# Kernel optimization log

Measured on AMD Instinct MI355X. Metric: run time of the kernel, lower is better.

## Reference

```python
import jax, jax.numpy as jnp
import numpy as np

NEG_SLOPE = 0.2  # PyG GATv2Conv default leaky_relu slope
N_NODES = 50000
N_EDGES = 800000
F_IN = 128
HID = 32
HEADS = 4
OUT_HEADS = 1
N_CLS = 16
MLP_HID = 128


def topk_mask(score, dst, k, num_nodes):
    """Boolean mask [E,H]: True where edge score is among top-k for its destination."""
    E = score.shape[0]
    counts = jnp.zeros((num_nodes,), jnp.int32).at[dst].add(1)
    starts = jnp.cumsum(counts) - counts  # first sorted index of each dst segment

    def one_head(s):
        o1 = jnp.argsort(-s)                       # sort by score desc
        o2 = jnp.argsort(dst[o1], stable=True)     # stable sort by dst -> (dst asc, score desc)
        perm = o1[o2]
        rank = jnp.arange(E) - starts[dst[perm]]   # rank within dst segment
        return jnp.zeros((E,), bool).at[perm].set(rank < k)

    return jax.vmap(one_head, in_axes=1, out_axes=1)(score)


def masked_segment_softmax(score, mask, dst, num_nodes):
    neg = jnp.where(mask, score, -jnp.inf)
    m = jax.ops.segment_max(neg, dst, num_segments=num_nodes)
    m = jnp.where(jnp.isfinite(m), m, 0.0)
    ex = jnp.where(mask, jnp.exp(score - m[dst]), 0.0)
    s = jax.ops.segment_sum(ex, dst, num_segments=num_nodes)
    return ex / (s[dst] + 1e-16)


def gatv2_topk(x, edge_index, k, Wl, Wr, att, b, heads, out_c, concat, num_nodes):
    src, dst = edge_index[0], edge_index[1]
    xl = (x @ Wl).reshape(num_nodes, heads, out_c)
    xr = (x @ Wr).reshape(num_nodes, heads, out_c)
    h = xl[src] + xr[dst]                                   # [E,H,C]
    e = jnp.einsum('ehc,hc->eh', jax.nn.leaky_relu(h, NEG_SLOPE), att)  # [E,H]
    keep = topk_mask(e, dst, k, num_nodes)
    alpha = masked_segment_softmax(e, keep, dst, num_nodes)       # top-k attention
    alpha_n = masked_segment_softmax(e, ~keep, dst, num_nodes)    # truncated (noise) attention
    msg = xl[src]                                                  # [E,H,C]
    out = jax.ops.segment_sum(alpha[..., None] * msg, dst, num_segments=num_nodes)
    noise = jax.ops.segment_sum(alpha_n[..., None] * msg, dst, num_segments=num_nodes)
    if concat:
        out = out.reshape(num_nodes, heads * out_c)
        noise = noise.reshape(num_nodes, heads * out_c)
    else:
        out = out.mean(axis=1)
        noise = noise.mean(axis=1)
    return out + b, noise + b


def setup_inputs() -> dict:
    key = jax.random.key(0)
    ks = jax.random.split(key, 14)
    s = 0.1
    x = jax.random.normal(ks[0], (N_NODES, F_IN), jnp.float32)
    edge_index = jax.random.randint(ks[1], (2, N_EDGES), 0, N_NODES, dtype=jnp.int64)
    return {
        'x': x,
        'edge_index': edge_index,
        'attn_topk': 8,
        'Wl1': jax.random.normal(ks[2], (F_IN, HEADS * HID), jnp.float32) * s,
        'Wr1': jax.random.normal(ks[3], (F_IN, HEADS * HID), jnp.float32) * s,
        'att1': jax.random.normal(ks[4], (HEADS, HID), jnp.float32) * s,
        'b1': jnp.zeros((HEADS * HID,), jnp.float32),
        'Wl2': jax.random.normal(ks[5], (HEADS * HID, OUT_HEADS * N_CLS), jnp.float32) * s,
        'Wr2': jax.random.normal(ks[6], (HEADS * HID, OUT_HEADS * N_CLS), jnp.float32) * s,
        'att2': jax.random.normal(ks[7], (OUT_HEADS, N_CLS), jnp.float32) * s,
        'b2': jnp.zeros((N_CLS,), jnp.float32),
        'lin1_w': jax.random.normal(ks[8], (HEADS * HID, MLP_HID), jnp.float32) * s,
        'lin1_b': jnp.zeros((MLP_HID,), jnp.float32),
        'lin2_w': jax.random.normal(ks[9], (MLP_HID, N_CLS), jnp.float32) * s,
        'lin2_b': jnp.zeros((N_CLS,), jnp.float32),
    }


def reference(x, edge_index, attn_topk, Wl1, Wr1, att1, b1, Wl2, Wr2, att2, b2,
              lin1_w, lin1_b, lin2_w, lin2_b):
    # eval mode: dropout is identity
    h, noise1 = gatv2_topk(x, edge_index, attn_topk, Wl1, Wr1, att1, b1,
                           HEADS, HID, True, N_NODES)
    h = jax.nn.elu(h)
    n1 = jax.nn.elu(noise1 @ lin1_w + lin1_b) @ lin2_w + lin2_b
    out, noise2 = gatv2_topk(h, edge_index, attn_topk, Wl2, Wr2, att2, b2,
                             OUT_HEADS, N_CLS, False, N_NODES)
    return (jax.nn.log_softmax(out, axis=1),
            jax.nn.log_softmax(n1, axis=1),
            jax.nn.log_softmax(noise2, axis=1))
```

## Files before the change

kernel.cpp:

```cpp
#include <hip/hip_runtime.h>
#include <math.h>

#define NN 50000
#define NE 800000
#define FIN 128
#define HEADS 4
#define HID 32
#define D1 128
#define NCLS 16
#define NEG 0.2f
#define NINF (-3.402823466e38f)
#define CAP 64
#define SB 256
#define NSB ((NN + SB - 1) / SB)

__global__ void k_count(const int* __restrict__ dst, int* __restrict__ counts) {
  int j = blockIdx.x * 256 + threadIdx.x;
  if (j < NE) atomicAdd(&counts[dst[j]], 1);
}

__global__ void k_scanA(const int* __restrict__ counts, int* __restrict__ bsum) {
  int b = blockIdx.x, t = threadIdx.x;
  int idx = b * SB + t;
  int v = idx < NN ? counts[idx] : 0;
  __shared__ int ws[4];
#pragma unroll
  for (int o = 1; o <= 32; o <<= 1) v += __shfl_xor(v, o, 64);
  if ((t & 63) == 0) ws[t >> 6] = v;
  __syncthreads();
  if (t == 0) bsum[b] = ws[0] + ws[1] + ws[2] + ws[3];
}

__global__ void k_scanB(const int* __restrict__ bsum, int* __restrict__ boff) {
  int t = threadIdx.x;
  int v = t < NSB ? bsum[t] : 0;
  __shared__ int tmp[256];
  tmp[t] = v;
  __syncthreads();
  for (int o = 1; o < 256; o <<= 1) {
    int u = t >= o ? tmp[t - o] : 0;
    __syncthreads();
    tmp[t] += u;
    __syncthreads();
  }
  if (t < NSB) boff[t] = tmp[t] - v;
}

__global__ void k_scanC(const int* __restrict__ counts, const int* __restrict__ boff,
                        int* __restrict__ starts, int* __restrict__ cursor) {
  int b = blockIdx.x, t = threadIdx.x;
  int idx = b * SB + t;
  int v = idx < NN ? counts[idx] : 0;
  __shared__ int tmp[256];
  tmp[t] = v;
  __syncthreads();
  for (int o = 1; o < 256; o <<= 1) {
    int u = t >= o ? tmp[t - o] : 0;
    __syncthreads();
    tmp[t] += u;
    __syncthreads();
  }
  int ex = tmp[t] - v + boff[b];
  if (idx < NN) { starts[idx] = ex; cursor[idx] = ex; }
}

__global__ void k_scatter(const int* __restrict__ src, const int* __restrict__ dst,
                          int* __restrict__ cursor, int* __restrict__ eperm,
                          int* __restrict__ sperm) {
  int j = blockIdx.x * 256 + threadIdx.x;
  if (j < NE) {
    int p = atomicAdd(&cursor[dst[j]], 1);
    eperm[p] = j;
    sperm[p] = src[j];
  }
}

template <int BM, int BN, int BK, int TM, int TN, int ACT>
__global__ __launch_bounds__(256) void k_gemm(const float* __restrict__ A,
                                              const float* __restrict__ B,
                                              const float* __restrict__ bias,
                                              float* __restrict__ C, int M, int N, int K) {
  constexpr int NT = (BM / TM) * (BN / TN);
  static_assert(NT == 256, "block must be 256 threads");
  __shared__ float As[BK][BM + 4];
  __shared__ float Bs[BK][BN];
  int tid = threadIdx.x;
  int bm = blockIdx.y * BM, bn = blockIdx.x * BN;
  constexpr int TX = BN / TN;
  int tn = (tid % TX) * TN;
  int tm = (tid / TX) * TM;
  float acc[TM][TN];
#pragma unroll
  for (int i = 0; i < TM; i++)
#pragma unroll
    for (int j = 0; j < TN; j++) acc[i][j] = 0.f;

  for (int k0 = 0; k0 < K; k0 += BK) {
    constexpr int AV = BM * BK / 4;
    for (int i = tid; i < AV; i += NT) {
      int r = i / (BK / 4);
      int c4 = (i % (BK / 4)) * 4;
      float4 v = make_float4(0.f, 0.f, 0.f, 0.f);
      int gr = bm + r;
      if (gr < M) v = *(const float4*)(A + (size_t)gr * K + k0 + c4);
      As[c4 + 0][r] = v.x; As[c4 + 1][r] = v.y; As[c4 + 2][r] = v.z; As[c4 + 3][r] = v.w;
    }
    constexpr int BV = BK * BN / 4;
    for (int i = tid; i < BV; i += NT) {
      int r = i / (BN / 4), c4 = (i % (BN / 4)) * 4;
      float4 v = *(const float4*)(B + (size_t)(k0 + r) * N + bn + c4);
      Bs[r][c4 + 0] = v.x; Bs[r][c4 + 1] = v.y; Bs[r][c4 + 2] = v.z; Bs[r][c4 + 3] = v.w;
    }
    __syncthreads();
#pragma unroll
    for (int kk = 0; kk < BK; kk++) {
      float ra[TM], rb[TN];
#pragma unroll
      for (int i = 0; i < TM; i++) ra[i] = As[kk][tm + i];
#pragma unroll
      for (int j = 0; j < TN; j++) rb[j] = Bs[kk][tn + j];
#pragma unroll
      for (int i = 0; i < TM; i++)
#pragma unroll
        for (int j = 0; j < TN; j++) acc[i][j] += ra[i] * rb[j];
    }
    __syncthreads();
  }
#pragma unroll
  for (int i = 0; i < TM; i++) {
    int gr = bm + tm + i;
    if (gr >= M) continue;
#pragma unroll
    for (int j = 0; j < TN; j++) {
      float v = acc[i][j];
      if (bias) v += bias[bn + tn + j];
      if (ACT == 1) v = v > 0.f ? v : expm1f(v);
      C[(size_t)gr * N + bn + tn + j] = v;
    }
  }
}

__device__ __forceinline__ bool lex_gt(float av, int ai, float bv, int bi) {
  return (av > bv) || (av == bv && ai < bi);
}

__global__ __launch_bounds__(256) void k_fused1(
    const float* __restrict__ xl, const float* __restrict__ xr,
    const float* __restrict__ att, const int* __restrict__ sperm,
    const int* __restrict__ eperm, const int* __restrict__ starts,
    const int* __restrict__ counts, const int* __restrict__ kptr,
    const float* __restrict__ bias, float* __restrict__ hout,
    float* __restrict__ nout) {
  __shared__ float sc[4][CAP][4];
  int w = threadIdx.x >> 6;
  int l = threadIdx.x & 63;
  int d = blockIdx.x * 4 + w;
  if (d >= NN) return;
  int st = starts[d];
  int deg = counts[d];
  if (deg > CAP) deg = CAP;
  int k = kptr[0];

  int srcreg = 0, idreg = 0x7fffffff;
  if (l < deg) { srcreg = sperm[st + l]; idreg = eperm[st + l]; }

  int h2 = l >> 5, li = l & 31;
  int headq = li >> 3;
  float4 xrv = *(const float4*)(xr + (size_t)d * D1 + 4 * li);
  float4 attv = *(const float4*)(att + 4 * li);
  float4 b1v = *(const float4*)(bias + 4 * li);

  for (int q = 0; q < deg; q += 4) {
    int r0 = q + h2, r1 = q + 2 + h2;
    int s0 = __shfl(srcreg, r0), s1 = __shfl(srcreg, r1);
    bool v0 = r0 < deg, v1 = r1 < deg;
    float4 x0 = make_float4(0.f, 0.f, 0.f, 0.f), x1 = x0;
    if (v0) x0 = *(const float4*)(xl + (size_t)s0 * D1 + 4 * li);
    if (v1) x1 = *(const float4*)(xl + (size_t)s1 * D1 + 4 * li);
    float a0, a1, p0 = 0.f, p1 = 0.f;
    a0 = x0.x + xrv.x; p0 += (a0 > 0.f ? a0 : NEG * a0) * attv.x;
    a0 = x0.y + xrv.y; p0 += (a0 > 0.f ? a0 : NEG * a0) * attv.y;
    a0 = x0.z + xrv.z; p0 += (a0 > 0.f ? a0 : NEG * a0) * attv.z;
    a0 = x0.w + xrv.w; p0 += (a0 > 0.f ? a0 : NEG * a0) * attv.w;
    a1 = x1.x + xrv.x; p1 += (a1 > 0.f ? a1 : NEG * a1) * attv.x;
    a1 = x1.y + xrv.y; p1 += (a1 > 0.f ? a1 : NEG * a1) * attv.y;
    a1 = x1.z + xrv.z; p1 += (a1 > 0.f ? a1 : NEG * a1) * attv.z;
    a1 = x1.w + xrv.w; p1 += (a1 > 0.f ? a1 : NEG * a1) * attv.w;
#pragma unroll
    for (int o = 1; o <= 4; o <<= 1) {
      p0 += __shfl_xor(p0, o, 64);
      p1 += __shfl_xor(p1, o, 64);
    }
    if ((li & 7) == 0) {
      if (v0) sc[w][r0][headq] = p0;
      if (v1) sc[w][r1][headq] = p1;
    }
  }

  int hh = l >> 4, ii = l & 15;
  float sv[4]; int si[4]; int rank[4]; bool val[4];
#pragma unroll
  for (int j = 0; j < 4; j++) {
    int q = j * 16 + ii;
    val[j] = q < deg;
    sv[j] = val[j] ? sc[w][q][hh] : NINF;
    int bid = __shfl(idreg, q);
    si[j] = val[j] ? bid : 0x7fffffff;
    rank[j] = 0;
  }
#pragma unroll
  for (int ch = 0; ch < 4; ch++) {
    if (ch * 16 >= deg) break;
#pragma unroll
    for (int pp = 0; pp < 16; pp++) {
      int p = ch * 16 + pp;
      float bv = __shfl(sv[ch], hh * 16 + pp);
      int bi = __shfl(si[ch], hh * 16 + pp);
      if (p < deg) {
#pragma unroll
        for (int j = 0; j < 4; j++) rank[j] += lex_gt(bv, bi, sv[j], si[j]);
      }
    }
  }
  bool kept[4];
#pragma unroll
  for (int j = 0; j < 4; j++) kept[j] = val[j] && (rank[j] < k);
  float mk = fmaxf(fmaxf(sv[0], sv[1]), fmaxf(sv[2], sv[3]));
  float mn = NINF;
#pragma unroll
  for (int j = 0; j < 4; j++) mn = fmaxf(mn, kept[j] ? NINF : sv[j]);
#pragma unroll
  for (int o = 1; o <= 8; o <<= 1) {
    mk = fmaxf(mk, __shfl_xor(mk, o, 64));
    mn = fmaxf(mn, __shfl_xor(mn, o, 64));
  }
  float ek[4], en[4], sk = 0.f, sn = 0.f;
#pragma unroll
  for (int j = 0; j < 4; j++) {
    ek[j] = kept[j] ? __expf(sv[j] - mk) : 0.f;
    en[j] = (val[j] && !kept[j]) ? __expf(sv[j] - mn) : 0.f;
    sk += ek[j]; sn += en[j];
  }
#pragma unroll
  for (int o = 1; o <= 8; o <<= 1) {
    sk += __shfl_xor(sk, o, 64);
    sn += __shfl_xor(sn, o, 64);
  }
  float ik = 1.f / (sk + 1e-16f), inn = 1.f / (sn + 1e-16f);
#pragma unroll
  for (int j = 0; j < 4; j++) {
    if (val[j]) sc[w][j * 16 + ii][hh] = kept[j] ? ek[j] * ik : -(en[j] * inn);
  }

  float4 ao = make_float4(0.f, 0.f, 0.f, 0.f), an = ao;
  for (int q = 0; q < deg; q += 4) {
    int r0 = q + h2, r1 = q + 2 + h2;
    int s0 = __shfl(srcreg, r0), s1 = __shfl(srcreg, r1);
    if (r0 < deg) {
      float wv = sc[w][r0][headq];
      float4 xv = *(const float4*)(xl + (size_t)s0 * D1 + 4 * li);
      float s = wv > 0.f ? wv : -wv;
      if (wv > 0.f) { ao.x += s * xv.x; ao.y += s * xv.y; ao.z += s * xv.z; ao.w += s * xv.w; }
      else          { an.x += s * xv.x; an.y += s * xv.y; an.z += s * xv.z; an.w += s * xv.w; }
    }
    if (r1 < deg) {
      float wv = sc[w][r1][headq];
      float4 xv = *(const float4*)(xl + (size_t)s1 * D1 + 4 * li);
      float s = wv > 0.f ? wv : -wv;
      if (wv > 0.f) { ao.x += s * xv.x; ao.y += s * xv.y; ao.z += s * xv.z; ao.w += s * xv.w; }
      else          { an.x += s * xv.x; an.y += s * xv.y; an.z += s * xv.z; an.w += s * xv.w; }
    }
  }
  ao.x += __shfl_xor(ao.x, 32, 64); ao.y += __shfl_xor(ao.y, 32, 64);
  ao.z += __shfl_xor(ao.z, 32, 64); ao.w += __shfl_xor(ao.w, 32, 64);
  an.x += __shfl_xor(an.x, 32, 64); an.y += __shfl_xor(an.y, 32, 64);
  an.z += __shfl_xor(an.z, 32, 64); an.w += __shfl_xor(an.w, 32, 64);
  if (h2 == 0) {
    float4 vo;
    vo.x = ao.x + b1v.x; vo.y = ao.y + b1v.y; vo.z = ao.z + b1v.z; vo.w = ao.w + b1v.w;
    vo.x = vo.x > 0.f ? vo.x : expm1f(vo.x);
    vo.y = vo.y > 0.f ? vo.y : expm1f(vo.y);
    vo.z = vo.z > 0.f ? vo.z : expm1f(vo.z);
    vo.w = vo.w > 0.f ? vo.w : expm1f(vo.w);
    *(float4*)(hout + (size_t)d * D1 + 4 * li) = vo;
  } else {
    float4 vn;
    vn.x = an.x + b1v.x; vn.y = an.y + b1v.y; vn.z = an.z + b1v.z; vn.w = an.w + b1v.w;
    *(float4*)(nout + (size_t)d * D1 + 4 * li) = vn;
  }
}

__global__ __launch_bounds__(256) void k_fused2(
    const float* __restrict__ xl, const float* __restrict__ xr,
    const float* __restrict__ att, const int* __restrict__ sperm,
    const int* __restrict__ eperm, const int* __restrict__ starts,
    const int* __restrict__ counts, const int* __restrict__ kptr,
    const float* __restrict__ bias, float* __restrict__ out0,
    float* __restrict__ out1) {
  __shared__ float sc[4][CAP];
  int w = threadIdx.x >> 6;
  int l = threadIdx.x & 63;
  int d = blockIdx.x * 4 + w;
  if (d >= NN) return;
  int st = starts[d];
  int deg = counts[d];
  if (deg > CAP) deg = CAP;
  int k = kptr[0];

  int srcreg = 0, idreg = 0x7fffffff;
  if (l < deg) { srcreg = sperm[st + l]; idreg = eperm[st + l]; }

  int g = l >> 4, li = l & 15;
  float xrv = xr[(size_t)d * NCLS + li];
  float attv = att[li];
  float bv2 = bias[li];

  for (int q = 0; q < deg; q += 8) {
    int r0 = q + g, r1 = q + 4 + g;
    int s0 = __shfl(srcreg, r0), s1 = __shfl(srcreg, r1);
    float x0 = (r0 < deg) ? xl[(size_t)s0 * NCLS + li] : 0.f;
    float x1 = (r1 < deg) ? xl[(size_t)s1 * NCLS + li] : 0.f;
    float a0 = x0 + xrv, a1 = x1 + xrv;
    float p0 = (a0 > 0.f ? a0 : NEG * a0) * attv;
    float p1 = (a1 > 0.f ? a1 : NEG * a1) * attv;
#pragma unroll
    for (int o = 1; o <= 8; o <<= 1) {
      p0 += __shfl_xor(p0, o, 64);
      p1 += __shfl_xor(p1, o, 64);
    }
    if (li == 0) {
      if (r0 < deg) sc[w][r0] = p0;
      if (r1 < deg) sc[w][r1] = p1;
    }
  }

  float sv = (l < deg) ? sc[w][l] : NINF;
  int si = idreg;
  int rank = 0;
  for (int p = 0; p < deg; p++) {
    float bv = __shfl(sv, p);
    int bi = __shfl(si, p);
    rank += lex_gt(bv, bi, sv, si);
  }
  bool kept = (l < deg) && (rank < k);
  float mk = sv, mn = kept ? NINF : sv;
#pragma unroll
  for (int o = 1; o <= 32; o <<= 1) {
    mk = fmaxf(mk, __shfl_xor(mk, o, 64));
    mn = fmaxf(mn, __shfl_xor(mn, o, 64));
  }
  float ek = kept ? __expf(sv - mk) : 0.f;
  float en = ((l < deg) && !kept) ? __expf(sv - mn) : 0.f;
  float sk = ek, sn = en;
#pragma unroll
  for (int o = 1; o <= 32; o <<= 1) {
    sk += __shfl_xor(sk, o, 64);
    sn += __shfl_xor(sn, o, 64);
  }
  if (l < deg) sc[w][l] = kept ? ek / (sk + 1e-16f) : -(en / (sn + 1e-16f));

  float ao = 0.f, an = 0.f;
  for (int q = 0; q < deg; q += 4) {
    int r = q + g;
    int s = __shfl(srcreg, r);
    if (r < deg) {
      float wv = sc[w][r];
      float xv = xl[(size_t)s * NCLS + li];
      if (wv > 0.f) ao += wv * xv; else an -= wv * xv;
    }
  }
  ao += __shfl_xor(ao, 16, 64); ao += __shfl_xor(ao, 32, 64);
  an += __shfl_xor(an, 16, 64); an += __shfl_xor(an, 32, 64);
  float vo = ao + bv2, vn = an + bv2;
  float mo = vo, mv = vn;
#pragma unroll
  for (int o = 1; o <= 8; o <<= 1) {
    mo = fmaxf(mo, __shfl_xor(mo, o, 64));
    mv = fmaxf(mv, __shfl_xor(mv, o, 64));
  }
  float eo = __expf(vo - mo), ev = __expf(vn - mv);
#pragma unroll
  for (int o = 1; o <= 8; o <<= 1) {
    eo += __shfl_xor(eo, o, 64);
    ev += __shfl_xor(ev, o, 64);
  }
  if (g == 0) out0[(size_t)d * NCLS + li] = vo - (mo + logf(eo));
  if (g == 1) out1[(size_t)d * NCLS + li] = vn - (mv + logf(ev));
}

__global__ void k_lsm(const float* __restrict__ in, float* __restrict__ out) {
  int r = blockIdx.x * 256 + threadIdx.x;
  if (r >= NN) return;
  const float4* p = (const float4*)(in + (size_t)r * NCLS);
  float4 a = p[0], b = p[1], c = p[2], d4 = p[3];
  float vals[16] = {a.x, a.y, a.z, a.w, b.x, b.y, b.z, b.w,
                    c.x, c.y, c.z, c.w, d4.x, d4.y, d4.z, d4.w};
  float m = vals[0];
#pragma unroll
  for (int i = 1; i < 16; i++) m = fmaxf(m, vals[i]);
  float s = 0.f;
#pragma unroll
  for (int i = 0; i < 16; i++) s += expf(vals[i] - m);
  float l = m + logf(s);
  float* op = out + (size_t)r * NCLS;
#pragma unroll
  for (int i = 0; i < 16; i++) op[i] = vals[i] - l;
}

extern "C" void kernel_launch(void* const* d_in, const int* in_sizes, int n_in,
                              void* d_out, int out_size, void* d_ws, size_t ws_size,
                              hipStream_t stream) {
  (void)in_sizes; (void)n_in; (void)out_size; (void)ws_size;
  const float* x    = (const float*)d_in[0];
  const int*   ei   = (const int*)d_in[1];
  const int*   kptr = (const int*)d_in[2];
  const float* Wl1  = (const float*)d_in[3];
  const float* Wr1  = (const float*)d_in[4];
  const float* att1 = (const float*)d_in[5];
  const float* b1   = (const float*)d_in[6];
  const float* Wl2  = (const float*)d_in[7];
  const float* Wr2  = (const float*)d_in[8];
  const float* att2 = (const float*)d_in[9];
  const float* b2   = (const float*)d_in[10];
  const float* l1w  = (const float*)d_in[11];
  const float* l1b  = (const float*)d_in[12];
  const float* l2w  = (const float*)d_in[13];
  const float* l2b  = (const float*)d_in[14];
  const int* srcv = ei;
  const int* dstv = ei + NE;

  char* wp = (char*)d_ws;
  auto alloc = [&](size_t n) { char* p = wp; wp += (n + 255) & ~(size_t)255; return p; };
  float* xl1    = (float*)alloc((size_t)NN * D1 * 4);
  float* bufB   = (float*)alloc((size_t)NN * D1 * 4);
  float* noise1 = (float*)alloc((size_t)NN * D1 * 4);
  float* t1     = (float*)alloc((size_t)NN * D1 * 4);
  int* counts = (int*)alloc((size_t)NN * 4);
  int* starts = (int*)alloc((size_t)NN * 4);
  int* cursor = (int*)alloc((size_t)NN * 4);
  int* eperm  = (int*)alloc((size_t)NE * 4);
  int* sperm  = (int*)alloc((size_t)NE * 4);
  int* bsum   = (int*)alloc((size_t)NSB * 4);
  int* boff   = (int*)alloc((size_t)NSB * 4);

  hipMemsetAsync(counts, 0, (size_t)NN * 4, stream);
  k_count<<<(NE + 255) / 256, 256, 0, stream>>>(dstv, counts);
  k_scanA<<<NSB, 256, 0, stream>>>(counts, bsum);
  k_scanB<<<1, 256, 0, stream>>>(bsum, boff);
  k_scanC<<<NSB, 256, 0, stream>>>(counts, boff, starts, cursor);
  k_scatter<<<(NE + 255) / 256, 256, 0, stream>>>(srcv, dstv, cursor, eperm, sperm);

  dim3 gbig(D1 / 64, (NN + 63) / 64);
  k_gemm<64, 64, 32, 4, 4, 0><<<gbig, 256, 0, stream>>>(x, Wl1, nullptr, xl1, NN, D1, FIN);
  k_gemm<64, 64, 32, 4, 4, 0><<<gbig, 256, 0, stream>>>(x, Wr1, nullptr, bufB, NN, D1, FIN);

  k_fused1<<<(NN + 3) / 4, 256, 0, stream>>>(xl1, bufB, att1, sperm, eperm,
                                             starts, counts, kptr, b1, bufB, noise1);

  k_gemm<64, 64, 32, 4, 4, 1><<<gbig, 256, 0, stream>>>(noise1, l1w, l1b, t1, NN, 128, 128);
  float* n1v = noise1;
  dim3 gsm(1, (NN + 127) / 128);
  k_gemm<128, 16, 32, 4, 2, 0><<<gsm, 256, 0, stream>>>(t1, l2w, l2b, n1v, NN, NCLS, 128);

  float* xl2 = t1;
  float* xr2 = t1 + (size_t)NN * NCLS;
  k_gemm<128, 16, 32, 4, 2, 0><<<gsm, 256, 0, stream>>>(bufB, Wl2, nullptr, xl2, NN, NCLS, D1);
  k_gemm<128, 16, 32, 4, 2, 0><<<gsm, 256, 0, stream>>>(bufB, Wr2, nullptr, xr2, NN, NCLS, D1);

  float* o = (float*)d_out;
  k_fused2<<<(NN + 3) / 4, 256, 0, stream>>>(xl2, xr2, att2, sperm, eperm, starts,
                                             counts, kptr, b2, o,
                                             o + (size_t)2 * NN * NCLS);

  k_lsm<<<(NN + 255) / 256, 256, 0, stream>>>(n1v, o + (size_t)NN * NCLS);
}
```

Baseline: 508.2 us.

## Fuse left/right projection GEMMs into one concatenated GEMM and vectorize fragments

```diff
diff --git a/kernel.cpp b/kernel.cpp
--- a/kernel.cpp
+++ b/kernel.cpp
@@ -76,12 +76,13 @@
 }
 
 template <int BM, int BN, int BK, int TM, int TN, int ACT>
-__global__ __launch_bounds__(256) void k_gemm(const float* __restrict__ A,
-                                              const float* __restrict__ B,
-                                              const float* __restrict__ bias,
-                                              float* __restrict__ C, int M, int N, int K) {
+__global__ __launch_bounds__(256) void k_gemm2(
+    const float* __restrict__ A, const float* __restrict__ B1,
+    const float* __restrict__ B2, int N1, int s1, int s2,
+    const float* __restrict__ bias, float* __restrict__ C, int M, int N, int K) {
   constexpr int NT = (BM / TM) * (BN / TN);
   static_assert(NT == 256, "block must be 256 threads");
+  static_assert(TM % 4 == 0 && TN % 4 == 0, "float4 fragments");
   __shared__ float As[BK][BM + 4];
   __shared__ float Bs[BK][BN];
   int tid = threadIdx.x;
@@ -108,7 +109,9 @@
     constexpr int BV = BK * BN / 4;
     for (int i = tid; i < BV; i += NT) {
       int r = i / (BN / 4), c4 = (i % (BN / 4)) * 4;
-      float4 v = *(const float4*)(B + (size_t)(k0 + r) * N + bn + c4);
+      int gc = bn + c4, gk = k0 + r;
+      float4 v = (gc < N1) ? *(const float4*)(B1 + (size_t)gk * s1 + gc)
+                           : *(const float4*)(B2 + (size_t)gk * s2 + (gc - N1));
       Bs[r][c4 + 0] = v.x; Bs[r][c4 + 1] = v.y; Bs[r][c4 + 2] = v.z; Bs[r][c4 + 3] = v.w;
     }
     __syncthreads();
@@ -116,9 +119,11 @@
     for (int kk = 0; kk < BK; kk++) {
       float ra[TM], rb[TN];
 #pragma unroll
-      for (int i = 0; i < TM; i++) ra[i] = As[kk][tm + i];
-#pragma unroll
-      for (int j = 0; j < TN; j++) rb[j] = Bs[kk][tn + j];
+      for (int i = 0; i < TM; i += 4)
+        *(float4*)&ra[i] = *(const float4*)&As[kk][tm + i];
+#pragma unroll
+      for (int j = 0; j < TN; j += 4)
+        *(float4*)&rb[j] = *(const float4*)&Bs[kk][tn + j];
 #pragma unroll
       for (int i = 0; i < TM; i++)
 #pragma unroll
@@ -131,11 +136,20 @@
     int gr = bm + tm + i;
     if (gr >= M) continue;
 #pragma unroll
-    for (int j = 0; j < TN; j++) {
-      float v = acc[i][j];
-      if (bias) v += bias[bn + tn + j];
-      if (ACT == 1) v = v > 0.f ? v : expm1f(v);
-      C[(size_t)gr * N + bn + tn + j] = v;
+    for (int j = 0; j < TN; j += 4) {
+      float4 v;
+      v.x = acc[i][j + 0]; v.y = acc[i][j + 1]; v.z = acc[i][j + 2]; v.w = acc[i][j + 3];
+      if (bias) {
+        v.x += bias[bn + tn + j + 0]; v.y += bias[bn + tn + j + 1];
+        v.z += bias[bn + tn + j + 2]; v.w += bias[bn + tn + j + 3];
+      }
+      if (ACT == 1) {
+        v.x = v.x > 0.f ? v.x : expm1f(v.x);
+        v.y = v.y > 0.f ? v.y : expm1f(v.y);
+        v.z = v.z > 0.f ? v.z : expm1f(v.z);
+        v.w = v.w > 0.f ? v.w : expm1f(v.w);
+      }
+      *(float4*)(C + (size_t)gr * N + bn + tn + j) = v;
     }
   }
 }
@@ -145,12 +159,11 @@
 }
 
 __global__ __launch_bounds__(256) void k_fused1(
-    const float* __restrict__ xl, const float* __restrict__ xr,
-    const float* __restrict__ att, const int* __restrict__ sperm,
-    const int* __restrict__ eperm, const int* __restrict__ starts,
-    const int* __restrict__ counts, const int* __restrict__ kptr,
-    const float* __restrict__ bias, float* __restrict__ hout,
-    float* __restrict__ nout) {
+    const float* __restrict__ xlr, const float* __restrict__ att,
+    const int* __restrict__ sperm, const int* __restrict__ eperm,
+    const int* __restrict__ starts, const int* __restrict__ counts,
+    const int* __restrict__ kptr, const float* __restrict__ bias,
+    float* __restrict__ hout, float* __restrict__ nout) {
   __shared__ float sc[4][CAP][4];
   int w = threadIdx.x >> 6;
   int l = threadIdx.x & 63;
@@ -166,34 +179,38 @@
 
   int h2 = l >> 5, li = l & 31;
   int headq = li >> 3;
-  float4 xrv = *(const float4*)(xr + (size_t)d * D1 + 4 * li);
+  float4 xrv = *(const float4*)(xlr + (size_t)d * 256 + 128 + 4 * li);
   float4 attv = *(const float4*)(att + 4 * li);
   float4 b1v = *(const float4*)(bias + 4 * li);
 
-  for (int q = 0; q < deg; q += 4) {
-    int r0 = q + h2, r1 = q + 2 + h2;
-    int s0 = __shfl(srcreg, r0), s1 = __shfl(srcreg, r1);
-    bool v0 = r0 < deg, v1 = r1 < deg;
-    float4 x0 = make_float4(0.f, 0.f, 0.f, 0.f), x1 = x0;
-    if (v0) x0 = *(const float4*)(xl + (size_t)s0 * D1 + 4 * li);
-    if (v1) x1 = *(const float4*)(xl + (size_t)s1 * D1 + 4 * li);
-    float a0, a1, p0 = 0.f, p1 = 0.f;
-    a0 = x0.x + xrv.x; p0 += (a0 > 0.f ? a0 : NEG * a0) * attv.x;
-    a0 = x0.y + xrv.y; p0 += (a0 > 0.f ? a0 : NEG * a0) * attv.y;
-    a0 = x0.z + xrv.z; p0 += (a0 > 0.f ? a0 : NEG * a0) * attv.z;
-    a0 = x0.w + xrv.w; p0 += (a0 > 0.f ? a0 : NEG * a0) * attv.w;
-    a1 = x1.x + xrv.x; p1 += (a1 > 0.f ? a1 : NEG * a1) * attv.x;
-    a1 = x1.y + xrv.y; p1 += (a1 > 0.f ? a1 : NEG * a1) * attv.y;
-    a1 = x1.z + xrv.z; p1 += (a1 > 0.f ? a1 : NEG * a1) * attv.z;
-    a1 = x1.w + xrv.w; p1 += (a1 > 0.f ? a1 : NEG * a1) * attv.w;
+  for (int q = 0; q < deg; q += 8) {
+    int rr[4]; int ssr[4]; bool vv[4]; float4 xv[4]; float pp[4];
+#pragma unroll
+    for (int j = 0; j < 4; j++) {
+      rr[j] = q + 2 * j + h2;
+      ssr[j] = __shfl(srcreg, rr[j]);
+      vv[j] = rr[j] < deg;
+      xv[j] = make_float4(0.f, 0.f, 0.f, 0.f);
+      if (vv[j]) xv[j] = *(const float4*)(xlr + (size_t)ssr[j] * 256 + 4 * li);
+    }
+#pragma unroll
+    for (int j = 0; j < 4; j++) {
+      float a, p = 0.f;
+      a = xv[j].x + xrv.x; p += fmaxf(a, NEG * a) * attv.x;
+      a = xv[j].y + xrv.y; p += fmaxf(a, NEG * a) * attv.y;
+      a = xv[j].z + xrv.z; p += fmaxf(a, NEG * a) * attv.z;
+      a = xv[j].w + xrv.w; p += fmaxf(a, NEG * a) * attv.w;
+      pp[j] = p;
+    }
 #pragma unroll
     for (int o = 1; o <= 4; o <<= 1) {
-      p0 += __shfl_xor(p0, o, 64);
-      p1 += __shfl_xor(p1, o, 64);
+#pragma unroll
+      for (int j = 0; j < 4; j++) pp[j] += __shfl_xor(pp[j], o, 64);
     }
     if ((li & 7) == 0) {
-      if (v0) sc[w][r0][headq] = p0;
-      if (v1) sc[w][r1][headq] = p1;
+#pragma unroll
+      for (int j = 0; j < 4; j++)
+        if (vv[j]) sc[w][rr[j]][headq] = pp[j];
     }
   }
 
@@ -258,17 +275,17 @@
     int s0 = __shfl(srcreg, r0), s1 = __shfl(srcreg, r1);
     if (r0 < deg) {
       float wv = sc[w][r0][headq];
-      float4 xv = *(const float4*)(xl + (size_t)s0 * D1 + 4 * li);
-      float s = wv > 0.f ? wv : -wv;
-      if (wv > 0.f) { ao.x += s * xv.x; ao.y += s * xv.y; ao.z += s * xv.z; ao.w += s * xv.w; }
-      else          { an.x += s * xv.x; an.y += s * xv.y; an.z += s * xv.z; an.w += s * xv.w; }
+      float pw = fmaxf(wv, 0.f), nw = pw - wv;
+      float4 xv = *(const float4*)(xlr + (size_t)s0 * 256 + 4 * li);
+      ao.x += pw * xv.x; ao.y += pw * xv.y; ao.z += pw * xv.z; ao.w += pw * xv.w;
+      an.x += nw * xv.x; an.y += nw * xv.y; an.z += nw * xv.z; an.w += nw * xv.w;
     }
     if (r1 < deg) {
       float wv = sc[w][r1][headq];
-      float4 xv = *(const float4*)(xl + (size_t)s1 * D1 + 4 * li);
-      float s = wv > 0.f ? wv : -wv;
-      if (wv > 0.f) { ao.x += s * xv.x; ao.y += s * xv.y; ao.z += s * xv.z; ao.w += s * xv.w; }
-      else          { an.x += s * xv.x; an.y += s * xv.y; an.z += s * xv.z; an.w += s * xv.w; }
+      float pw = fmaxf(wv, 0.f), nw = pw - wv;
+      float4 xv = *(const float4*)(xlr + (size_t)s1 * 256 + 4 * li);
+      ao.x += pw * xv.x; ao.y += pw * xv.y; ao.z += pw * xv.z; ao.w += pw * xv.w;
+      an.x += nw * xv.x; an.y += nw * xv.y; an.z += nw * xv.z; an.w += nw * xv.w;
     }
   }
   ao.x += __shfl_xor(ao.x, 32, 64); ao.y += __shfl_xor(ao.y, 32, 64);
@@ -291,12 +308,11 @@
 }
 
 __global__ __launch_bounds__(256) void k_fused2(
-    const float* __restrict__ xl, const float* __restrict__ xr,
-    const float* __restrict__ att, const int* __restrict__ sperm,
-    const int* __restrict__ eperm, const int* __restrict__ starts,
-    const int* __restrict__ counts, const int* __restrict__ kptr,
-    const float* __restrict__ bias, float* __restrict__ out0,
-    float* __restrict__ out1) {
+    const float* __restrict__ xlr, const float* __restrict__ att,
+    const int* __restrict__ sperm, const int* __restrict__ eperm,
+    const int* __restrict__ starts, const int* __restrict__ counts,
+    const int* __restrict__ kptr, const float* __restrict__ bias,
+    float* __restrict__ out0, float* __restrict__ out1) {
   __shared__ float sc[4][CAP];
   int w = threadIdx.x >> 6;
   int l = threadIdx.x & 63;
@@ -311,18 +327,18 @@
   if (l < deg) { srcreg = sperm[st + l]; idreg = eperm[st + l]; }
 
   int g = l >> 4, li = l & 15;
-  float xrv = xr[(size_t)d * NCLS + li];
+  float xrv = xlr[(size_t)d * 32 + 16 + li];
   float attv = att[li];
   float bv2 = bias[li];
 
   for (int q = 0; q < deg; q += 8) {
     int r0 = q + g, r1 = q + 4 + g;
     int s0 = __shfl(srcreg, r0), s1 = __shfl(srcreg, r1);
-    float x0 = (r0 < deg) ? xl[(size_t)s0 * NCLS + li] : 0.f;
-    float x1 = (r1 < deg) ? xl[(size_t)s1 * NCLS + li] : 0.f;
+    float x0 = (r0 < deg) ? xlr[(size_t)s0 * 32 + li] : 0.f;
+    float x1 = (r1 < deg) ? xlr[(size_t)s1 * 32 + li] : 0.f;
     float a0 = x0 + xrv, a1 = x1 + xrv;
-    float p0 = (a0 > 0.f ? a0 : NEG * a0) * attv;
-    float p1 = (a1 > 0.f ? a1 : NEG * a1) * attv;
+    float p0 = fmaxf(a0, NEG * a0) * attv;
+    float p1 = fmaxf(a1, NEG * a1) * attv;
 #pragma unroll
     for (int o = 1; o <= 8; o <<= 1) {
       p0 += __shfl_xor(p0, o, 64);
@@ -365,8 +381,9 @@
     int s = __shfl(srcreg, r);
     if (r < deg) {
       float wv = sc[w][r];
-      float xv = xl[(size_t)s * NCLS + li];
-      if (wv > 0.f) ao += wv * xv; else an -= wv * xv;
+      float pw = fmaxf(wv, 0.f), nw = pw - wv;
+      float xv = xlr[(size_t)s * 32 + li];
+      ao += pw * xv; an += nw * xv;
     }
   }
   ao += __shfl_xor(ao, 16, 64); ao += __shfl_xor(ao, 32, 64);
@@ -431,10 +448,12 @@
 
   char* wp = (char*)d_ws;
   auto alloc = [&](size_t n) { char* p = wp; wp += (n + 255) & ~(size_t)255; return p; };
-  float* xl1    = (float*)alloc((size_t)NN * D1 * 4);
-  float* bufB   = (float*)alloc((size_t)NN * D1 * 4);
+  float* xlr1   = (float*)alloc((size_t)NN * 256 * 4);
+  float* hbuf   = (float*)alloc((size_t)NN * D1 * 4);
   float* noise1 = (float*)alloc((size_t)NN * D1 * 4);
   float* t1     = (float*)alloc((size_t)NN * D1 * 4);
+  float* xlr2   = (float*)alloc((size_t)NN * 32 * 4);
+  float* n1buf  = (float*)alloc((size_t)NN * NCLS * 4);
   int* counts = (int*)alloc((size_t)NN * 4);
   int* starts = (int*)alloc((size_t)NN * 4);
   int* cursor = (int*)alloc((size_t)NN * 4);
@@ -450,27 +469,24 @@
   k_scanC<<<NSB, 256, 0, stream>>>(counts, boff, starts, cursor);
   k_scatter<<<(NE + 255) / 256, 256, 0, stream>>>(srcv, dstv, cursor, eperm, sperm);
 
-  dim3 gbig(D1 / 64, (NN + 63) / 64);
-  k_gemm<64, 64, 32, 4, 4, 0><<<gbig, 256, 0, stream>>>(x, Wl1, nullptr, xl1, NN, D1, FIN);
-  k_gemm<64, 64, 32, 4, 4, 0><<<gbig, 256, 0, stream>>>(x, Wr1, nullptr, bufB, NN, D1, FIN);
-
-  k_fused1<<<(NN + 3) / 4, 256, 0, stream>>>(xl1, bufB, att1, sperm, eperm,
-                                             starts, counts, kptr, b1, bufB, noise1);
-
-  k_gemm<64, 64, 32, 4, 4, 1><<<gbig, 256, 0, stream>>>(noise1, l1w, l1b, t1, NN, 128, 128);
-  float* n1v = noise1;
-  dim3 gsm(1, (NN + 127) / 128);
-  k_gemm<128, 16, 32, 4, 2, 0><<<gsm, 256, 0, stream>>>(t1, l2w, l2b, n1v, NN, NCLS, 128);
-
-  float* xl2 = t1;
-  float* xr2 = t1 + (size_t)NN * NCLS;
-  k_gemm<128, 16, 32, 4, 2, 0><<<gsm, 256, 0, stream>>>(bufB, Wl2, nullptr, xl2, NN, NCLS, D1);
-  k_gemm<128, 16, 32, 4, 2, 0><<<gsm, 256, 0, stream>>>(bufB, Wr2, nullptr, xr2, NN, NCLS, D1);
+  k_gemm2<64, 128, 32, 4, 8, 0><<<dim3(2, (NN + 63) / 64), 256, 0, stream>>>(
+      x, Wl1, Wr1, 128, 128, 128, nullptr, xlr1, NN, 256, FIN);
+
+  k_fused1<<<(NN + 3) / 4, 256, 0, stream>>>(xlr1, att1, sperm, eperm,
+                                             starts, counts, kptr, b1, hbuf, noise1);
+
+  k_gemm2<64, 128, 32, 4, 8, 1><<<dim3(1, (NN + 63) / 64), 256, 0, stream>>>(
+      noise1, l1w, l1w, 128, 128, 128, l1b, t1, NN, 128, 128);
+  k_gemm2<256, 16, 32, 4, 4, 0><<<dim3(1, (NN + 255) / 256), 256, 0, stream>>>(
+      t1, l2w, l2w, 16, 16, 16, l2b, n1buf, NN, NCLS, 128);
+
+  k_gemm2<128, 32, 32, 4, 4, 0><<<dim3(1, (NN + 127) / 128), 256, 0, stream>>>(
+      hbuf, Wl2, Wr2, 16, 16, 16, nullptr, xlr2, NN, 32, D1);
 
   float* o = (float*)d_out;
-  k_fused2<<<(NN + 3) / 4, 256, 0, stream>>>(xl2, xr2, att2, sperm, eperm, starts,
+  k_fused2<<<(NN + 3) / 4, 256, 0, stream>>>(xlr2, att2, sperm, eperm, starts,
                                              counts, kptr, b2, o,
                                              o + (size_t)2 * NN * NCLS);
 
-  k_lsm<<<(NN + 255) / 256, 256, 0, stream>>>(n1v, o + (size_t)NN * NCLS);
-}
+  k_lsm<<<(NN + 255) / 256, 256, 0, stream>>>(n1buf, o + (size_t)NN * NCLS);
+}
```

Result: faster. 488.6 us (-3.9%).
